# Kernel tuning notes

Hardware: AMD Instinct MI355X
Metric: run time of the kernel (lower is better)

## Reference

```python
import jax, jax.numpy as jnp
import numpy as np

T, B, DI, DL, V = 1024, 128, 256, 512, 10000


def setup_inputs() -> dict:
    key = jax.random.key(0)
    ks = jax.random.split(key, 6)
    return {
        "X": jax.random.randint(ks[0], (T, B), 0, V, dtype=jnp.int64),
        "h0": jnp.zeros((B, DL), dtype=jnp.float32),
        "emb": jax.random.normal(ks[1], (V, DI), dtype=jnp.float32),
        "Wi": jax.random.normal(ks[2], (DI, DL), dtype=jnp.float32) * (1.0 / np.sqrt(DI)),
        "bi": jax.random.normal(ks[3], (DL,), dtype=jnp.float32) * 0.02,
        "Wh": jax.random.normal(ks[4], (DL, DL), dtype=jnp.float32) * (1.0 / np.sqrt(DL)),
        "bh": jax.random.normal(ks[5], (DL,), dtype=jnp.float32) * 0.02,
    }


def reference(X, h0, emb, Wi, bi, Wh, bh):
    # Elman RNN: h_t = tanh(W_i emb(x_t) + b_i + W_h h_{t-1} + b_h)
    Xe = emb[X]                              # [T, B, DI] embedding lookup
    pre = jnp.einsum("tbd,dl->tbl", Xe, Wi) + bi  # input projections, batched over time

    def step(h, p):
        h_new = jnp.tanh(p + h @ Wh + bh)
        return h_new, h_new

    _, H = jax.lax.scan(step, h0, pre)       # H: [T, B, DL]
    return H
```

## Files before the change

### kernel.cpp

```cpp
#include <hip/hip_runtime.h>
#include <math.h>

typedef _Float16 f16;
typedef _Float16 f16x8 __attribute__((ext_vector_type(8)));
typedef float f32x4 __attribute__((ext_vector_type(4)));

#define T_ 1024
#define B_ 128
#define DI_ 256
#define DL_ 512
#define V_ 10000

#define OFF_EMBH   0u
#define OFF_WIT    5120000u
#define OFF_WFRAG  5382144u
#define OFF_BSUM   5906432u

__device__ __forceinline__ float fast_tanh(float x) {
  float e = __builtin_amdgcn_exp2f(x * 2.88539008177793f);
  return 1.f - 2.f * __builtin_amdgcn_rcpf(e + 1.f);
}

__global__ void prep_emb_k(const float* __restrict__ emb, f16* __restrict__ embH, int n) {
  for (int i = blockIdx.x * blockDim.x + threadIdx.x; i < n; i += gridDim.x * blockDim.x)
    embH[i] = (f16)emb[i];
}

__global__ void prep_w_k(const float* __restrict__ Wi, const float* __restrict__ Wh,
                         const float* __restrict__ bi, const float* __restrict__ bh,
                         f16* __restrict__ WiT, f16* __restrict__ Wfrag,
                         float* __restrict__ bsum) {
  int i = blockIdx.x * blockDim.x + threadIdx.x;
  if (i < 131072) {
    int n = i & 511, k = i >> 9;
    WiT[n * 256 + k] = (f16)Wi[k * 512 + n];
  } else if (i < 131072 + 32768) {
    int s = i - 131072;
    int l = s & 63, kk = (s >> 6) & 15, ct = s >> 10;
    int n = ct * 16 + (l & 15);
    int kbase = kk * 32 + (l >> 4) * 8;
    f16 tmp[8];
#pragma unroll
    for (int e = 0; e < 8; e++) tmp[e] = (f16)Wh[(size_t)(kbase + e) * 512 + n];
    *(f16x8*)&Wfrag[(size_t)s * 8] = *(f16x8*)tmp;
  } else if (i < 131072 + 32768 + 512) {
    int s = i - 131072 - 32768;
    bsum[s] = bi[s] + bh[s];
  }
}

__global__ __launch_bounds__(256) void gemmA_k(
    const int* __restrict__ X, const f16* __restrict__ embH,
    const f16* __restrict__ WiT, const float* __restrict__ bsum,
    float* __restrict__ out) {
  __shared__ f16 Ah[128][40];
  __shared__ f16 Bh[128][40];
  __shared__ int idxL[128];

  int tid = threadIdx.x;
  int lane = tid & 63, w = tid >> 6;
  int wr = w >> 1, wc = w & 1;
  int by = blockIdx.y, bx = blockIdx.x;
  int m0 = by * 128, n0 = bx * 128;

  if (tid < 128) {
    int v = X[m0 + tid];
    idxL[tid] = (v < 0) ? 0 : ((v >= V_) ? (V_ - 1) : v);
  }
  __syncthreads();

  f32x4 acc[4][4];
#pragma unroll
  for (int i = 0; i < 4; i++)
#pragma unroll
    for (int jj = 0; jj < 4; jj++) acc[i][jj] = (f32x4){0.f, 0.f, 0.f, 0.f};

  int ar = lane & 15, koff = (lane >> 4) * 8;

  for (int kk = 0; kk < 8; kk++) {
    int k0 = kk * 32;
#pragma unroll
    for (int q = 0; q < 2; q++) {
      int s = tid + 256 * q;
      int row = s >> 2, part = s & 3;
      *(uint4*)&Ah[row][part * 8] = *(const uint4*)&embH[idxL[row] * 256 + k0 + part * 8];
      *(uint4*)&Bh[row][part * 8] = *(const uint4*)&WiT[(n0 + row) * 256 + k0 + part * 8];
    }
    __syncthreads();
    f16x8 a[4], b[4];
#pragma unroll
    for (int i = 0; i < 4; i++) a[i] = *(const f16x8*)&Ah[wr * 64 + i * 16 + ar][koff];
#pragma unroll
    for (int jj = 0; jj < 4; jj++) b[jj] = *(const f16x8*)&Bh[wc * 64 + jj * 16 + ar][koff];
#pragma unroll
    for (int i = 0; i < 4; i++)
#pragma unroll
      for (int jj = 0; jj < 4; jj++)
        acc[i][jj] = __builtin_amdgcn_mfma_f32_16x16x32_f16(a[i], b[jj], acc[i][jj], 0, 0, 0);
    __syncthreads();
  }

#pragma unroll
  for (int i = 0; i < 4; i++) {
#pragma unroll
    for (int jj = 0; jj < 4; jj++) {
      int c = wr * 4 + i;
      int ct = bx * 8 + wc * 4 + jj;
      float bs = bsum[ct * 16 + ar];
      f32x4 v = acc[i][jj];
      v[0] += bs; v[1] += bs; v[2] += bs; v[3] += bs;
      *(f32x4*)&out[(size_t)by * 65536 + (size_t)c * 8192 + ct * 256 + lane * 4] = v;
    }
  }
}

__global__ __launch_bounds__(512, 2) void rnnB_k(
    const float* __restrict__ h0, const f16* __restrict__ Wfrag,
    float* __restrict__ H) {
  __shared__ f16 Wlds[8 * 16 * 64 * 8];
  __shared__ f16 hA[16 * 64 * 8];

  int tid = threadIdx.x, lane = tid & 63, w = tid >> 6;
  int c = blockIdx.x;
  int w4 = w * 4;
  int ar = lane & 15, r0 = (lane >> 4) * 4;

  const f16x8* Wfr = (const f16x8*)Wfrag;

  for (int idx = tid; idx < 8192; idx += 512) {
    int l = idx & 63, kk = (idx >> 6) & 15, s = idx >> 10;
    *(f16x8*)&Wlds[(size_t)idx * 8] = Wfr[((s * 4 + 3) * 16 + kk) * 64 + l];
  }
  for (int idx = tid; idx < 8192; idx += 512) {
    int kk = idx >> 9, l = (idx >> 3) & 63, e = idx & 7;
    int row = l & 15, k = kk * 32 + (l >> 4) * 8 + e;
    hA[idx] = (f16)h0[(size_t)(c * 16 + row) * 512 + k];
  }

  f16x8 Wreg[48];
#pragma unroll
  for (int ti = 0; ti < 3; ti++)
#pragma unroll
    for (int kk = 0; kk < 16; kk++)
      Wreg[ti * 16 + kk] = Wfr[((w4 + ti) * 16 + kk) * 64 + lane];

  f32x4 pre[4];
  {
    const f32x4* preb = (const f32x4*)(H + (size_t)c * 8192);
#pragma unroll
    for (int ti = 0; ti < 4; ti++) pre[ti] = preb[(w4 + ti) * 64 + lane];
  }

  for (int t = 0; t < 1024; t++) {
    __syncthreads();

    f32x4 acc[4];
#pragma unroll
    for (int ti = 0; ti < 4; ti++) acc[ti] = (f32x4){0.f, 0.f, 0.f, 0.f};

#pragma unroll
    for (int kk = 0; kk < 16; kk++) {
      f16x8 a = *(const f16x8*)&hA[(size_t)(kk * 64 + lane) * 8];
      f16x8 w3 = *(const f16x8*)&Wlds[(size_t)((w * 16 + kk) * 64 + lane) * 8];
      acc[0] = __builtin_amdgcn_mfma_f32_16x16x32_f16(a, Wreg[0 * 16 + kk], acc[0], 0, 0, 0);
      acc[1] = __builtin_amdgcn_mfma_f32_16x16x32_f16(a, Wreg[1 * 16 + kk], acc[1], 0, 0, 0);
      acc[2] = __builtin_amdgcn_mfma_f32_16x16x32_f16(a, Wreg[2 * 16 + kk], acc[2], 0, 0, 0);
      acc[3] = __builtin_amdgcn_mfma_f32_16x16x32_f16(a, w3, acc[3], 0, 0, 0);
    }

    __syncthreads();

    float* Hblk = H + (size_t)t * 65536 + (size_t)c * 8192;
#pragma unroll
    for (int ti = 0; ti < 4; ti++) {
      int ct = w4 + ti;
      int kkA = ct >> 1;
#pragma unroll
      for (int r = 0; r < 4; r++) {
        float v = fast_tanh(acc[ti][r] + pre[ti][r]);
        Hblk[(size_t)(r0 + r) * 512 + ct * 16 + ar] = v;
        int lA = (r0 + r) | ((((ct & 1) << 1) | (ar >> 3)) << 4);
        hA[((kkA * 64 + lA) << 3) + (ar & 7)] = (f16)v;
      }
    }

    int tn = (t < 1023) ? t + 1 : 0;
    const f32x4* preb = (const f32x4*)(H + (size_t)tn * 65536 + (size_t)c * 8192);
#pragma unroll
    for (int ti = 0; ti < 4; ti++) pre[ti] = preb[(w4 + ti) * 64 + lane];
  }
}

extern "C" void kernel_launch(void* const* d_in, const int* in_sizes, int n_in,
                              void* d_out, int out_size, void* d_ws, size_t ws_size,
                              hipStream_t stream) {
  const int* X     = (const int*)d_in[0];
  const float* h0  = (const float*)d_in[1];
  const float* emb = (const float*)d_in[2];
  const float* Wi  = (const float*)d_in[3];
  const float* bi  = (const float*)d_in[4];
  const float* Wh  = (const float*)d_in[5];
  const float* bh  = (const float*)d_in[6];
  float* H = (float*)d_out;

  char* ws = (char*)d_ws;
  f16* embH   = (f16*)(ws + OFF_EMBH);
  f16* WiT    = (f16*)(ws + OFF_WIT);
  f16* Wfrag  = (f16*)(ws + OFF_WFRAG);
  float* bsum = (float*)(ws + OFF_BSUM);

  prep_emb_k<<<2560, 256, 0, stream>>>(emb, embH, V_ * DI_);
  prep_w_k<<<642, 256, 0, stream>>>(Wi, Wh, bi, bh, WiT, Wfrag, bsum);
  gemmA_k<<<dim3(4, 1024), 256, 0, stream>>>(X, embH, WiT, bsum, H);
  rnnB_k<<<8, 512, 0, stream>>>(h0, Wfrag, H);
}
```

Before: 3.469 ms.

## Stream one Wh column tile from global and prefetch pre-activations mid-step

The recurrent kernel now keeps only two column tiles of Wh in registers and one in LDS. The fourth tile is streamed from global memory (expected to hit L2) through a 4-deep rotating register buffer during the MFMA loop. The next step's pre-activation loads are issued inside the MFMA loop rather than after the tanh/store phase, and the time loop is unrolled by two to ping-pong the pre buffers. This is meant to lower register pressure and hide load latency on the serial critical path. The cost is an extra global load per MFMA on every step, and the pre-activation prefetch reads H slots that this kernel overwrites, which relies on step ordering.

After: 4.482 ms. 29.2% more time.

```diff
diff --git a/kernel.cpp b/kernel.cpp
--- a/kernel.cpp
+++ b/kernel.cpp
@@ -114,6 +114,45 @@
   }
 }
 
+#define RNN_STEP(T, PCUR, PNXT)                                               \
+  {                                                                           \
+    __syncthreads();          \
+    f32x4 acc[4] = {{0.f,0.f,0.f,0.f},{0.f,0.f,0.f,0.f},                      \
+                    {0.f,0.f,0.f,0.f},{0.f,0.f,0.f,0.f}};                     \
+    int tn_ = (T) + 1; if (tn_ >= 1024) tn_ = 0;      \
+    const f32x4* pb_ = (const f32x4*)(H + (size_t)tn_ * 65536 + (size_t)c * 8192); \
+    _Pragma("unroll")                                                         \
+    for (int kk = 0; kk < 16; kk++) {                                         \
+      f16x8 a_  = *(const f16x8*)&hA[(kk * 64 + lane) * 8];                   \
+      f16x8 wl_ = *(const f16x8*)&Wlds[((w * 16 + kk) * 64 + lane) * 8];      \
+      acc[0] = __builtin_amdgcn_mfma_f32_16x16x32_f16(a_, Wreg[kk],      acc[0], 0, 0, 0); \
+      acc[1] = __builtin_amdgcn_mfma_f32_16x16x32_f16(a_, Wreg[16 + kk], acc[1], 0, 0, 0); \
+      acc[2] = __builtin_amdgcn_mfma_f32_16x16x32_f16(a_, wl_,           acc[2], 0, 0, 0); \
+      acc[3] = __builtin_amdgcn_mfma_f32_16x16x32_f16(a_, ws[kk & 3],    acc[3], 0, 0, 0); \
+      ws[kk & 3] = Wfr[sbase + (((kk + 4) & 15) << 6)];  \
+      if (kk == 2) {                                                          \
+        PNXT[0] = pb_[(w4 + 0) * 64 + lane];                                  \
+        PNXT[1] = pb_[(w4 + 1) * 64 + lane];                                  \
+        PNXT[2] = pb_[(w4 + 2) * 64 + lane];                                  \
+        PNXT[3] = pb_[(w4 + 3) * 64 + lane];                                  \
+      }                                                                       \
+    }                                                                         \
+    __syncthreads();         \
+    float* Hblk_ = H + (size_t)(T) * 65536 + (size_t)c * 8192;                \
+    _Pragma("unroll")                                                         \
+    for (int ti = 0; ti < 4; ti++) {                                          \
+      int ct_ = w4 + ti;                                                      \
+      int base_ = ((ct_ >> 1) * 64) << 3;                                     \
+      int hi_ = (((ct_ & 1) << 1) | (ar >> 3)) << 4;                          \
+      _Pragma("unroll")                                                       \
+      for (int r = 0; r < 4; r++) {                                           \
+        float v_ = fast_tanh(acc[ti][r] + PCUR[ti][r]);                       \
+        Hblk_[(size_t)(r0 + r) * 512 + ct_ * 16 + ar] = v_;                   \
+        hA[base_ + (((r0 + r) | hi_) << 3) + (ar & 7)] = (f16)v_;             \
+      }                                                                       \
+    }                                                                         \
+  }
+
 __global__ __launch_bounds__(512, 2) void rnnB_k(
     const float* __restrict__ h0, const f16* __restrict__ Wfrag,
     float* __restrict__ H) {
@@ -129,7 +168,7 @@
 
   for (int idx = tid; idx < 8192; idx += 512) {
     int l = idx & 63, kk = (idx >> 6) & 15, s = idx >> 10;
-    *(f16x8*)&Wlds[(size_t)idx * 8] = Wfr[((s * 4 + 3) * 16 + kk) * 64 + l];
+    *(f16x8*)&Wlds[(size_t)idx * 8] = Wfr[((s * 4 + 2) * 16 + kk) * 64 + l];
   }
   for (int idx = tid; idx < 8192; idx += 512) {
     int kk = idx >> 9, l = (idx >> 3) & 63, e = idx & 7;
@@ -137,57 +176,28 @@
     hA[idx] = (f16)h0[(size_t)(c * 16 + row) * 512 + k];
   }
 
-  f16x8 Wreg[48];
-#pragma unroll
-  for (int ti = 0; ti < 3; ti++)
+  f16x8 Wreg[32];
+#pragma unroll
+  for (int ti = 0; ti < 2; ti++)
 #pragma unroll
     for (int kk = 0; kk < 16; kk++)
       Wreg[ti * 16 + kk] = Wfr[((w4 + ti) * 16 + kk) * 64 + lane];
 
-  f32x4 pre[4];
+  int sbase = ((w4 + 3) * 16) * 64 + lane;
+  f16x8 ws[4];
+#pragma unroll
+  for (int i = 0; i < 4; i++) ws[i] = Wfr[sbase + (i << 6)];
+
+  f32x4 preA[4], preB[4];
   {
-    const f32x4* preb = (const f32x4*)(H + (size_t)c * 8192);
-#pragma unroll
-    for (int ti = 0; ti < 4; ti++) pre[ti] = preb[(w4 + ti) * 64 + lane];
-  }
-
-  for (int t = 0; t < 1024; t++) {
-    __syncthreads();
-
-    f32x4 acc[4];
-#pragma unroll
-    for (int ti = 0; ti < 4; ti++) acc[ti] = (f32x4){0.f, 0.f, 0.f, 0.f};
-
-#pragma unroll
-    for (int kk = 0; kk < 16; kk++) {
-      f16x8 a = *(const f16x8*)&hA[(size_t)(kk * 64 + lane) * 8];
-      f16x8 w3 = *(const f16x8*)&Wlds[(size_t)((w * 16 + kk) * 64 + lane) * 8];
-      acc[0] = __builtin_amdgcn_mfma_f32_16x16x32_f16(a, Wreg[0 * 16 + kk], acc[0], 0, 0, 0);
-      acc[1] = __builtin_amdgcn_mfma_f32_16x16x32_f16(a, Wreg[1 * 16 + kk], acc[1], 0, 0, 0);
-      acc[2] = __builtin_amdgcn_mfma_f32_16x16x32_f16(a, Wreg[2 * 16 + kk], acc[2], 0, 0, 0);
-      acc[3] = __builtin_amdgcn_mfma_f32_16x16x32_f16(a, w3, acc[3], 0, 0, 0);
-    }
-
-    __syncthreads();
-
-    float* Hblk = H + (size_t)t * 65536 + (size_t)c * 8192;
-#pragma unroll
-    for (int ti = 0; ti < 4; ti++) {
-      int ct = w4 + ti;
-      int kkA = ct >> 1;
-#pragma unroll
-      for (int r = 0; r < 4; r++) {
-        float v = fast_tanh(acc[ti][r] + pre[ti][r]);
-        Hblk[(size_t)(r0 + r) * 512 + ct * 16 + ar] = v;
-        int lA = (r0 + r) | ((((ct & 1) << 1) | (ar >> 3)) << 4);
-        hA[((kkA * 64 + lA) << 3) + (ar & 7)] = (f16)v;
-      }
-    }
-
-    int tn = (t < 1023) ? t + 1 : 0;
-    const f32x4* preb = (const f32x4*)(H + (size_t)tn * 65536 + (size_t)c * 8192);
-#pragma unroll
-    for (int ti = 0; ti < 4; ti++) pre[ti] = preb[(w4 + ti) * 64 + lane];
+    const f32x4* pb = (const f32x4*)(H + (size_t)c * 8192);
+#pragma unroll
+    for (int ti = 0; ti < 4; ti++) preA[ti] = pb[(w4 + ti) * 64 + lane];
+  }
+
+  for (int s = 0; s < 512; s++) {
+    RNN_STEP(2 * s,     preA, preB)
+    RNN_STEP(2 * s + 1, preB, preA)
   }
 }
 
```
